# Performance work log

Hardware: AMD Instinct MI355X
Metric: run time of the kernel (lower is better)

Reference implementation:

```python
import jax, jax.numpy as jnp
import numpy as np

N_REGIONS = 17
N_CH = 7
ROWS, COLS = 82, 67
N_CELLS = 3000
BATCH = 2048


def setup_inputs() -> dict:
    key = jax.random.key(0)
    k1, k2 = jax.random.split(key)
    x = jax.random.normal(k1, (BATCH, N_REGIONS * N_CH), dtype=jnp.float32)
    # distinct linear cell indices -> unique (row, col) pairs
    cell_lin = jnp.arange(N_CELLS, dtype=jnp.int64)
    region_ids = jax.random.randint(k2, (N_CELLS,), 0, N_REGIONS, dtype=jnp.int64)
    return {"x": x, "cell_lin": cell_lin, "region_ids": region_ids}


def reference(x, cell_lin, region_ids):
    B = x.shape[0]
    reshaped = x.reshape(B, N_REGIONS, N_CH)          # (B, 17, 7)
    rows = cell_lin // COLS                           # (M,)
    cols = cell_lin % COLS                            # (M,)
    updates = reshaped[:, region_ids, :]              # (B, M, 7) gather per cell
    out = jnp.zeros((B, ROWS, COLS, N_CH), dtype=x.dtype)
    out = out.at[rows, cols].set(updates.transpose(1, 0, 2).reshape(N_CELLS, B, N_CH).transpose(0, 1, 2), mode="drop") if False else out.at[:, rows, cols, :].set(updates)
    return out
```

## Files before the change

### kernel.cpp

```cpp
#include <hip/hip_runtime.h>

#define N_REGIONS 17
#define N_CH 7
#define ROWS_ 82
#define COLS_ 67
#define N_MAP (ROWS_ * COLS_)
#define ELEMS_PER_B (N_MAP * N_CH)

__global__ void init_map_k(int* __restrict__ map) {
    int i = blockIdx.x * blockDim.x + threadIdx.x;
    if (i < N_MAP) map[i] = -1;
}

__global__ void scatter_map_k(const int* __restrict__ cell_lin,
                              const int* __restrict__ region_ids,
                              int n, int* __restrict__ map) {
    int i = blockIdx.x * blockDim.x + threadIdx.x;
    if (i < n) {
        int c = cell_lin[i];
        if (c >= 0 && c < N_MAP) map[c] = region_ids[i];
    }
}

__global__ __launch_bounds__(256) void fill_k(const float* __restrict__ x,
                                              const int* __restrict__ map,
                                              float* __restrict__ out,
                                              unsigned total4) {
    unsigned stride = gridDim.x * blockDim.x;
    for (unsigned t = blockIdx.x * blockDim.x + threadIdx.x; t < total4; t += stride) {
        unsigned e0 = t * 4u;
        float4 v;
        float* vp = reinterpret_cast<float*>(&v);
#pragma unroll
        for (int j = 0; j < 4; ++j) {
            unsigned e = e0 + (unsigned)j;
            unsigned b = e / ELEMS_PER_B;
            unsigned rem = e - b * ELEMS_PER_B;
            unsigned cell = rem / N_CH;
            unsigned ch = rem - cell * N_CH;
            int reg = map[cell];
            vp[j] = (reg >= 0) ? x[b * (N_REGIONS * N_CH) + reg * N_CH + ch] : 0.0f;
        }
        *reinterpret_cast<float4*>(out + e0) = v;
    }
}

extern "C" void kernel_launch(void* const* d_in, const int* in_sizes, int n_in,
                              void* d_out, int out_size, void* d_ws, size_t ws_size,
                              hipStream_t stream) {
    const float* x        = (const float*)d_in[0];
    const int* cell_lin   = (const int*)d_in[1];
    const int* region_ids = (const int*)d_in[2];
    float* out = (float*)d_out;
    int* map = (int*)d_ws;
    int n_cells = in_sizes[1];

    init_map_k<<<(N_MAP + 255) / 256, 256, 0, stream>>>(map);
    scatter_map_k<<<(n_cells + 255) / 256, 256, 0, stream>>>(cell_lin, region_ids, n_cells, map);

    unsigned total4 = (unsigned)out_size / 4u;
    fill_k<<<2048, 256, 0, stream>>>(x, map, out, total4);
}
```

Measured before the change: 73.15 us.

## Precompute per-element source-offset table over batch pairs and stream output nontemporally

Replaces the per-cell region map with a short-typed table of source offsets for every output element across two batch rows. The fill kernel then needs one division and one short4 load per four outputs instead of four divisions and four map lookups, and it writes with nontemporal stores. EPB (38458) is not a multiple of 4, which is why the table spans a pair of batches. That keeps each float4 group inside one table period, at the cost of a larger table (about 154 KB) to initialise and scatter.

```diff
diff --git a/kernel.cpp b/kernel.cpp
--- a/kernel.cpp
+++ b/kernel.cpp
@@ -5,43 +5,52 @@
 #define ROWS_ 82
 #define COLS_ 67
 #define N_MAP (ROWS_ * COLS_)
-#define ELEMS_PER_B (N_MAP * N_CH)
+#define EPB (N_MAP * N_CH)
+#define PAIR (2 * EPB)
+#define XROW (N_REGIONS * N_CH)
 
-__global__ void init_map_k(int* __restrict__ map) {
+typedef float f32x4 __attribute__((ext_vector_type(4)));
+
+
+__global__ void init_table_k(short* __restrict__ t) {
     int i = blockIdx.x * blockDim.x + threadIdx.x;
-    if (i < N_MAP) map[i] = -1;
+    if (i < PAIR) t[i] = -1;
 }
 
-__global__ void scatter_map_k(const int* __restrict__ cell_lin,
-                              const int* __restrict__ region_ids,
-                              int n, int* __restrict__ map) {
+__global__ void scatter_table_k(const int* __restrict__ cell_lin,
+                                const int* __restrict__ region_ids,
+                                int n, short* __restrict__ t) {
     int i = blockIdx.x * blockDim.x + threadIdx.x;
-    if (i < n) {
-        int c = cell_lin[i];
-        if (c >= 0 && c < N_MAP) map[c] = region_ids[i];
+    if (i >= n) return;
+    int c = cell_lin[i];
+    int r = region_ids[i];
+    if (c < 0 || c >= N_MAP) return;
+#pragma unroll
+    for (int lb = 0; lb < 2; ++lb) {
+        int dst = lb * EPB + c * N_CH;
+        short src = (short)(lb * XROW + r * N_CH);
+#pragma unroll
+        for (int ch = 0; ch < N_CH; ++ch) t[dst + ch] = (short)(src + ch);
     }
 }
 
-__global__ __launch_bounds__(256) void fill_k(const float* __restrict__ x,
-                                              const int* __restrict__ map,
-                                              float* __restrict__ out,
-                                              unsigned total4) {
+__global__ __launch_bounds__(256) void fill2_k(const float* __restrict__ x,
+                                               const short* __restrict__ t,
+                                               float* __restrict__ out,
+                                               unsigned total4) {
     unsigned stride = gridDim.x * blockDim.x;
-    for (unsigned t = blockIdx.x * blockDim.x + threadIdx.x; t < total4; t += stride) {
-        unsigned e0 = t * 4u;
-        float4 v;
-        float* vp = reinterpret_cast<float*>(&v);
-#pragma unroll
-        for (int j = 0; j < 4; ++j) {
-            unsigned e = e0 + (unsigned)j;
-            unsigned b = e / ELEMS_PER_B;
-            unsigned rem = e - b * ELEMS_PER_B;
-            unsigned cell = rem / N_CH;
-            unsigned ch = rem - cell * N_CH;
-            int reg = map[cell];
-            vp[j] = (reg >= 0) ? x[b * (N_REGIONS * N_CH) + reg * N_CH + ch] : 0.0f;
-        }
-        *reinterpret_cast<float4*>(out + e0) = v;
+    for (unsigned i = blockIdx.x * blockDim.x + threadIdx.x; i < total4; i += stride) {
+        unsigned e0 = i * 4u;
+        unsigned p = e0 / PAIR;
+        unsigned off = e0 - p * PAIR;
+        short4 s = *reinterpret_cast<const short4*>(t + off);
+        const float* xb = x + p * (2 * XROW);
+        f32x4 v;
+        v.x = (s.x >= 0) ? xb[s.x] : 0.0f;
+        v.y = (s.y >= 0) ? xb[s.y] : 0.0f;
+        v.z = (s.z >= 0) ? xb[s.z] : 0.0f;
+        v.w = (s.w >= 0) ? xb[s.w] : 0.0f;
+        __builtin_nontemporal_store(v, reinterpret_cast<f32x4*>(out + e0));
     }
 }
 
@@ -52,12 +61,12 @@
     const int* cell_lin   = (const int*)d_in[1];
     const int* region_ids = (const int*)d_in[2];
     float* out = (float*)d_out;
-    int* map = (int*)d_ws;
+    short* table = (short*)d_ws;
     int n_cells = in_sizes[1];
 
-    init_map_k<<<(N_MAP + 255) / 256, 256, 0, stream>>>(map);
-    scatter_map_k<<<(n_cells + 255) / 256, 256, 0, stream>>>(cell_lin, region_ids, n_cells, map);
+    init_table_k<<<(PAIR + 255) / 256, 256, 0, stream>>>(table);
+    scatter_table_k<<<(n_cells + 255) / 256, 256, 0, stream>>>(cell_lin, region_ids, n_cells, table);
 
     unsigned total4 = (unsigned)out_size / 4u;
-    fill_k<<<2048, 256, 0, stream>>>(x, map, out, total4);
+    fill2_k<<<2048, 256, 0, stream>>>(x, table, out, total4);
 }
```

After: 72.96 us. Within noise of the previous version (-0.3%).
